# Kernel tuning notes

Hardware: AMD Instinct MI355X
Metric: run time of the kernel (lower is better)

## Reference

```python
import jax, jax.numpy as jnp
import numpy as np

# ---- constants derived from init_kwargs ----
DETECT_THRESHOLD = 3.0
DETECT_SIGN = -1          # negative spikes
MARGIN_LEFT = 20          # snippet_T1
MARGIN_RIGHT = 20         # snippet_T2
CHANNEL_RADIUS = 100.0
SAMPLING_FREQUENCY = 30000.0
TIME_RADIUS = int(np.ceil(0.5 / 1000.0 * SAMPLING_FREQUENCY))  # = 15
MAX_DETECTIONS = 100000   # static cap for jit-compatible compaction


def setup_inputs() -> dict:
    key = jax.random.key(0)
    k1, k2 = jax.random.split(key)
    traces = jax.random.normal(k1, (150000, 384), dtype=jnp.float32)
    # spread channels over a 2000x2000 um area so radius=100 gives sparse adjacency
    channel_locations = jax.random.uniform(k2, (384, 2), dtype=jnp.float32) * 2000.0
    return {"traces": traces, "channel_locations": channel_locations}


def _detect_mask(traces, channel_locations):
    N, M = traces.shape
    # orientation (detect_sign < 0 -> traces_inv = -traces)
    if DETECT_SIGN > 0:
        traces_inv = traces
    elif DETECT_SIGN == 0:
        traces_inv = jnp.abs(traces)
    else:
        traces_inv = -traces

    # temporal max-pool, kernel 2*TR+1, stride 1, same padding (pads with -inf)
    pool = 2 * TIME_RADIUS + 1
    neg_inf = jnp.float32(-jnp.inf)
    temporal_max = jax.lax.reduce_window(
        traces_inv, neg_inf, jax.lax.max,
        window_dimensions=(pool, 1), window_strides=(1, 1),
        padding=((TIME_RADIUS, TIME_RADIUS), (0, 0)))  # [N, M]

    # channel adjacency from pairwise distances
    diff = channel_locations[:, None, :] - channel_locations[None, :, :]
    dists = jnp.sqrt(jnp.sum(diff * diff, axis=-1))  # [M, M]
    adj = dists <= CHANNEL_RADIUS

    # per-channel masked neighbor max over temporal_max columns -> [N, M]
    # sequential lax.map over channels avoids an N x M x M intermediate
    spatial_max = jax.lax.map(
        lambda row: jnp.max(jnp.where(row[None, :], temporal_max, neg_inf), axis=1),
        adj).T  # [N, M]

    t = jnp.arange(N)
    margin_ok = (t >= MARGIN_LEFT) & (t < N - MARGIN_RIGHT)  # [N]

    valid = ((traces_inv == temporal_max)
             & (traces_inv >= DETECT_THRESHOLD)
             & margin_ok[:, None]
             & (traces_inv >= spatial_max))
    return valid, traces_inv


def reference(traces, channel_locations):
    valid, _ = _detect_mask(traces, channel_locations)
    # row-major nonzero order == stable sort by time (row index)
    times, chans = jnp.nonzero(valid, size=MAX_DETECTIONS, fill_value=-1)
    return times.astype(jnp.int64), chans.astype(jnp.int32)
```

## Files before the change

### kernel.cpp

```cpp
#include <hip/hip_runtime.h>
#include <stdint.h>

#define M_CH       384
#define TR         15
#define MARGIN     20
#define CHUNK_ROWS 16
#define BM_WORDS   192
#define WPR        12

__device__ __forceinline__ uint32_t spread4(uint32_t x) {
    x = (x | (x << 12)) & 0x000F000Fu;
    x = (x | (x << 6))  & 0x03030303u;
    x = (x | (x << 3))  & 0x11111111u;
    return x;
}

__global__ void nbr_kernel(const float* __restrict__ locs,
                           uint32_t* __restrict__ nEntries,
                           uint8_t* __restrict__ entryWord,
                           uint32_t* __restrict__ entryMask) {
    __shared__ float lx[M_CH], ly[M_CH];
    int t = threadIdx.x;
    lx[t] = locs[2 * t];
    ly[t] = locs[2 * t + 1];
    __syncthreads();
    float x = lx[t], y = ly[t];
    uint32_t m[WPR];
    #pragma unroll
    for (int k = 0; k < WPR; ++k) m[k] = 0;
    for (int c = 0; c < M_CH; ++c) {
        float dx = x - lx[c], dy = y - ly[c];
        if (sqrtf(dx * dx + dy * dy) <= 100.0f) m[c >> 5] |= 1u << (c & 31);
    }
    int ne = 0;
    #pragma unroll
    for (int k = 0; k < WPR; ++k) {
        if (m[k]) {
            entryWord[t * WPR + ne] = (uint8_t)k;
            entryMask[t * WPR + ne] = m[k];
            ne++;
        }
    }
    nEntries[t] = (uint32_t)ne;
}

__global__ __launch_bounds__(256)
void cand_kernel(const float* __restrict__ traces, long n4, long nwords,
                 uint32_t* __restrict__ candWords) {
    const int lane = threadIdx.x & 63;
    const long stride = (long)gridDim.x * 256;
    for (long i = (long)blockIdx.x * 256 + threadIdx.x; i - lane < n4; i += stride) {
        float4 v = make_float4(0.f, 0.f, 0.f, 0.f);
        if (i < n4) v = ((const float4*)traces)[i];
        uint64_t B0 = __ballot(v.x <= -3.0f);
        uint64_t B1 = __ballot(v.y <= -3.0f);
        uint64_t B2 = __ballot(v.z <= -3.0f);
        uint64_t B3 = __ballot(v.w <= -3.0f);
        if (lane < 8) {
            uint32_t b0 = (uint32_t)(B0 >> (8 * lane)) & 0xFFu;
            uint32_t b1 = (uint32_t)(B1 >> (8 * lane)) & 0xFFu;
            uint32_t b2 = (uint32_t)(B2 >> (8 * lane)) & 0xFFu;
            uint32_t b3 = (uint32_t)(B3 >> (8 * lane)) & 0xFFu;
            uint32_t word = spread4(b0) | (spread4(b1) << 1)
                          | (spread4(b2) << 2) | (spread4(b3) << 3);
            long wIdx = (i - lane) / 8 + lane;
            if (wIdx < nwords) candWords[wIdx] = word;
        }
    }
}

__global__ __launch_bounds__(256)
void validate_kernel(const float* __restrict__ traces, int N, long nwords,
                     const uint32_t* __restrict__ nEntries,
                     const uint8_t* __restrict__ entryWord,
                     const uint32_t* __restrict__ entryMask,
                     const uint32_t* __restrict__ candWords,
                     uint32_t* __restrict__ validOut) {
    long w = (long)blockIdx.x * 256 + threadIdx.x;
    if (w >= nwords) return;
    uint32_t word = candWords[w];
    uint32_t out = 0;
    if (word) {
        int r  = (int)(w / WPR);
        int cw = (int)(w - (long)r * WPR);
        if (r >= MARGIN && r < N - MARGIN) {
            out = word;
            uint32_t tmp = word;
            while (tmp) {
                int bit = __ffs(tmp) - 1;
                tmp &= tmp - 1;
                int c = cw * 32 + bit;
                float raw = traces[(long)r * M_CH + c];
                int ne = (int)nEntries[c];
                bool bad = false;
                for (int k = 0; k < ne; ++k) {
                    int wi = (int)entryWord[c * WPR + k];
                    uint32_t em = entryMask[c * WPR + k];
                    const uint32_t* colp = candWords + (long)(r - TR) * WPR + wi;
                    uint32_t hitRows = 0;
                    #pragma unroll
                    for (int dt = 0; dt < 31; ++dt) {
                        uint32_t h = colp[(long)dt * WPR] & em;
                        hitRows |= (h ? 1u : 0u) << dt;
                    }
                    if (hitRows) {
                        while (hitRows) {
                            int dt = __ffs(hitRows) - 1;
                            hitRows &= hitRows - 1;
                            uint32_t h = colp[(long)dt * WPR] & em;
                            while (h) {
                                int b2 = __ffs(h) - 1;
                                h &= h - 1;
                                float v = traces[(long)(r - TR + dt) * M_CH + wi * 32 + b2];
                                if (v < raw) bad = true;
                            }
                        }
                        if (bad) break;
                    }
                }
                if (bad) out &= ~(1u << bit);
            }
        }
    }
    validOut[w] = out;
}

__global__ void count_kernel(const uint32_t* __restrict__ validOut, int nchunk,
                             uint32_t* __restrict__ chunkCounts) {
    int lane  = threadIdx.x & 63;
    int chunk = (blockIdx.x * blockDim.x + threadIdx.x) >> 6;
    if (chunk >= nchunk) return;
    const uint32_t* wp = validOut + (long)chunk * BM_WORDS;
    int s = __popc(wp[lane]) + __popc(wp[lane + 64]) + __popc(wp[lane + 128]);
    #pragma unroll
    for (int off = 32; off; off >>= 1) s += __shfl_xor(s, off, 64);
    if (lane == 0) chunkCounts[chunk] = (uint32_t)s;
}

__global__ void scan_kernel(const uint32_t* __restrict__ counts, int n,
                            uint32_t* __restrict__ prefix) {
    __shared__ uint32_t s[256];
    int t = threadIdx.x;
    int per = (n + 255) / 256;
    int lo = t * per, hi = min(lo + per, n);
    uint32_t sum = 0;
    for (int i = lo; i < hi; ++i) sum += counts[i];
    s[t] = sum;
    __syncthreads();
    for (int off = 1; off < 256; off <<= 1) {
        uint32_t v = (t >= off) ? s[t - off] : 0;
        __syncthreads();
        s[t] += v;
        __syncthreads();
    }
    uint32_t run = s[t] - sum;
    for (int i = lo; i < hi; ++i) { prefix[i] = run; run += counts[i]; }
    if (t == 255) prefix[n] = run;
}

__global__ void emit_kernel(const uint32_t* __restrict__ validOut,
                            const uint32_t* __restrict__ chunkPrefix,
                            int nchunk, int maxdet,
                            int* __restrict__ times, int* __restrict__ chans) {
    int wv = threadIdx.x >> 6;
    int lane = threadIdx.x & 63;
    int chunkId = blockIdx.x * 4 + wv;
    if (chunkId >= nchunk) return;

    const uint32_t* wp = validOut + (long)chunkId * BM_WORDS + lane * 3;
    uint32_t b0 = wp[0], b1 = wp[1], b2 = wp[2];
    int local = __popc(b0) + __popc(b1) + __popc(b2);

    int s = local;
    #pragma unroll
    for (int off = 1; off < 64; off <<= 1) {
        int v = __shfl_up(s, off, 64);
        if (lane >= off) s += v;
    }
    int base = (int)chunkPrefix[chunkId] + (s - local);
    int r0 = chunkId * CHUNK_ROWS;

    uint32_t words[3] = { b0, b1, b2 };
    #pragma unroll
    for (int q = 0; q < 3; ++q) {
        uint32_t x = words[q];
        int fbase = (lane * 3 + q) * 32;
        while (x) {
            int b = __ffs(x) - 1;
            x &= x - 1;
            int f = fbase + b;
            int n = f / M_CH;
            int ch = f - n * M_CH;
            if (base < maxdet) {
                times[base] = r0 + n;
                chans[base] = ch;
            }
            base++;
        }
    }
}

__global__ void fill_kernel(const uint32_t* __restrict__ totalPtr, int maxdet,
                            int* __restrict__ times, int* __restrict__ chans) {
    int i = blockIdx.x * blockDim.x + threadIdx.x;
    int total = (int)*totalPtr;
    if (i < maxdet && i >= total) { times[i] = -1; chans[i] = -1; }
}

extern "C" void kernel_launch(void* const* d_in, const int* in_sizes, int n_in,
                              void* d_out, int out_size, void* d_ws, size_t ws_size,
                              hipStream_t stream) {
    const float* traces = (const float*)d_in[0];
    const float* locs   = (const float*)d_in[1];
    const int M = M_CH;
    const int N = in_sizes[0] / M;
    const long nsamp = (long)N * M;
    const int maxdet = out_size / 2;
    int* times = (int*)d_out;
    int* chans = times + maxdet;

    const long n4     = nsamp / 4;
    const long nwords = nsamp / 32;
    const int  nchunk = (N + CHUNK_ROWS - 1) / CHUNK_ROWS;

    char* ws = (char*)d_ws;
    uint32_t* nEntries    = (uint32_t*)(ws + 0);
    uint8_t*  entryWord   = (uint8_t*)(ws + 1536);
    uint32_t* entryMask   = (uint32_t*)(ws + 6144);
    uint32_t* chunkCounts = (uint32_t*)(ws + 24576);
    uint32_t* chunkPrefix = (uint32_t*)(ws + 62080);
    uint32_t* candWords   = (uint32_t*)(ws + 99584);
    uint32_t* validOut    = (uint32_t*)(ws + 7299584);

    nbr_kernel<<<1, M_CH, 0, stream>>>(locs, nEntries, entryWord, entryMask);

    cand_kernel<<<2048, 256, 0, stream>>>(traces, n4, nwords, candWords);

    validate_kernel<<<(int)((nwords + 255) / 256), 256, 0, stream>>>(
        traces, N, nwords, nEntries, entryWord, entryMask, candWords, validOut);

    count_kernel<<<(nchunk * 64 + 255) / 256, 256, 0, stream>>>(validOut, nchunk,
                                                                chunkCounts);

    scan_kernel<<<1, 256, 0, stream>>>(chunkCounts, nchunk, chunkPrefix);

    emit_kernel<<<(nchunk + 3) / 4, 256, 0, stream>>>(validOut, chunkPrefix,
                                                      nchunk, maxdet,
                                                      times, chans);

    fill_kernel<<<(maxdet + 255) / 256, 256, 0, stream>>>(chunkPrefix + nchunk,
                                                          maxdet, times, chans);
}
```

Before: 428.1 us.

## Fuse validate with chunk counting, emit with fill, and widen cand_kernel loads

The per-chunk popcount is folded into the validate kernel, which now runs one 192-thread block per 16-row chunk and reduces counts in shared memory. The fill pass is merged into the emit kernel as extra blocks. The candidate kernel switches from a grid-stride loop to one pass per wave that issues four float4 loads before balloting. Together these drop two kernel launches and one re-read of validOut, at the cost of smaller validate blocks and one more barrier.

```diff
diff --git a/kernel.cpp b/kernel.cpp
--- a/kernel.cpp
+++ b/kernel.cpp
@@ -48,93 +48,109 @@
 void cand_kernel(const float* __restrict__ traces, long n4, long nwords,
                  uint32_t* __restrict__ candWords) {
     const int lane = threadIdx.x & 63;
-    const long stride = (long)gridDim.x * 256;
-    for (long i = (long)blockIdx.x * 256 + threadIdx.x; i - lane < n4; i += stride) {
-        float4 v = make_float4(0.f, 0.f, 0.f, 0.f);
-        if (i < n4) v = ((const float4*)traces)[i];
-        uint64_t B0 = __ballot(v.x <= -3.0f);
-        uint64_t B1 = __ballot(v.y <= -3.0f);
-        uint64_t B2 = __ballot(v.z <= -3.0f);
-        uint64_t B3 = __ballot(v.w <= -3.0f);
-        if (lane < 8) {
-            uint32_t b0 = (uint32_t)(B0 >> (8 * lane)) & 0xFFu;
-            uint32_t b1 = (uint32_t)(B1 >> (8 * lane)) & 0xFFu;
-            uint32_t b2 = (uint32_t)(B2 >> (8 * lane)) & 0xFFu;
-            uint32_t b3 = (uint32_t)(B3 >> (8 * lane)) & 0xFFu;
-            uint32_t word = spread4(b0) | (spread4(b1) << 1)
-                          | (spread4(b2) << 2) | (spread4(b3) << 3);
-            long wIdx = (i - lane) / 8 + lane;
-            if (wIdx < nwords) candWords[wIdx] = word;
-        }
-    }
-}
-
-__global__ __launch_bounds__(256)
-void validate_kernel(const float* __restrict__ traces, int N, long nwords,
-                     const uint32_t* __restrict__ nEntries,
-                     const uint8_t* __restrict__ entryWord,
-                     const uint32_t* __restrict__ entryMask,
-                     const uint32_t* __restrict__ candWords,
-                     uint32_t* __restrict__ validOut) {
-    long w = (long)blockIdx.x * 256 + threadIdx.x;
-    if (w >= nwords) return;
-    uint32_t word = candWords[w];
+    const long wv = (((long)blockIdx.x * 256) + threadIdx.x) >> 6;
+    const long fb = wv * 256;
+    uint64_t B00,B01,B02,B03, B10,B11,B12,B13,
+             B20,B21,B22,B23, B30,B31,B32,B33;
+    {
+        float4 v0 = make_float4(0,0,0,0), v1 = v0, v2 = v0, v3 = v0;
+        long i0 = fb + 0 * 64 + lane;
+        long i1 = fb + 1 * 64 + lane;
+        long i2 = fb + 2 * 64 + lane;
+        long i3 = fb + 3 * 64 + lane;
+        if (i0 < n4) v0 = ((const float4*)traces)[i0];
+        if (i1 < n4) v1 = ((const float4*)traces)[i1];
+        if (i2 < n4) v2 = ((const float4*)traces)[i2];
+        if (i3 < n4) v3 = ((const float4*)traces)[i3];
+        B00 = __ballot(v0.x <= -3.0f); B01 = __ballot(v0.y <= -3.0f);
+        B02 = __ballot(v0.z <= -3.0f); B03 = __ballot(v0.w <= -3.0f);
+        B10 = __ballot(v1.x <= -3.0f); B11 = __ballot(v1.y <= -3.0f);
+        B12 = __ballot(v1.z <= -3.0f); B13 = __ballot(v1.w <= -3.0f);
+        B20 = __ballot(v2.x <= -3.0f); B21 = __ballot(v2.y <= -3.0f);
+        B22 = __ballot(v2.z <= -3.0f); B23 = __ballot(v2.w <= -3.0f);
+        B30 = __ballot(v3.x <= -3.0f); B31 = __ballot(v3.y <= -3.0f);
+        B32 = __ballot(v3.z <= -3.0f); B33 = __ballot(v3.w <= -3.0f);
+    }
+    if (lane < 32) {
+        int k  = lane >> 3;
+        int sh = (lane & 7) * 8;
+        uint64_t b0 = (k & 2) ? ((k & 1) ? B30 : B20) : ((k & 1) ? B10 : B00);
+        uint64_t b1 = (k & 2) ? ((k & 1) ? B31 : B21) : ((k & 1) ? B11 : B01);
+        uint64_t b2 = (k & 2) ? ((k & 1) ? B32 : B22) : ((k & 1) ? B12 : B02);
+        uint64_t b3 = (k & 2) ? ((k & 1) ? B33 : B23) : ((k & 1) ? B13 : B03);
+        uint32_t w = spread4((uint32_t)(b0 >> sh) & 0xFFu)
+                   | (spread4((uint32_t)(b1 >> sh) & 0xFFu) << 1)
+                   | (spread4((uint32_t)(b2 >> sh) & 0xFFu) << 2)
+                   | (spread4((uint32_t)(b3 >> sh) & 0xFFu) << 3);
+        long wIdx = wv * 32 + lane;
+        if (wIdx < nwords) candWords[wIdx] = w;
+    }
+}
+
+__global__ __launch_bounds__(192)
+void validate_count_kernel(const float* __restrict__ traces, int N, long nwords,
+                           const uint32_t* __restrict__ nEntries,
+                           const uint8_t* __restrict__ entryWord,
+                           const uint32_t* __restrict__ entryMask,
+                           const uint32_t* __restrict__ candWords,
+                           uint32_t* __restrict__ validOut,
+                           uint32_t* __restrict__ chunkCounts) {
+    __shared__ uint32_t red[3];
+    const int t = threadIdx.x;
+    const long w = (long)blockIdx.x * BM_WORDS + t;
     uint32_t out = 0;
-    if (word) {
-        int r  = (int)(w / WPR);
-        int cw = (int)(w - (long)r * WPR);
-        if (r >= MARGIN && r < N - MARGIN) {
-            out = word;
-            uint32_t tmp = word;
-            while (tmp) {
-                int bit = __ffs(tmp) - 1;
-                tmp &= tmp - 1;
-                int c = cw * 32 + bit;
-                float raw = traces[(long)r * M_CH + c];
-                int ne = (int)nEntries[c];
-                bool bad = false;
-                for (int k = 0; k < ne; ++k) {
-                    int wi = (int)entryWord[c * WPR + k];
-                    uint32_t em = entryMask[c * WPR + k];
-                    const uint32_t* colp = candWords + (long)(r - TR) * WPR + wi;
-                    uint32_t hitRows = 0;
-                    #pragma unroll
-                    for (int dt = 0; dt < 31; ++dt) {
-                        uint32_t h = colp[(long)dt * WPR] & em;
-                        hitRows |= (h ? 1u : 0u) << dt;
+    if (w < nwords) {
+        uint32_t word = candWords[w];
+        if (word) {
+            int r  = (int)(w / WPR);
+            int cw = (int)(w - (long)r * WPR);
+            if (r >= MARGIN && r < N - MARGIN) {
+                out = word;
+                uint32_t tmp = word;
+                while (tmp) {
+                    int bit = __ffs(tmp) - 1;
+                    tmp &= tmp - 1;
+                    int c = cw * 32 + bit;
+                    float raw = traces[(long)r * M_CH + c];
+                    int ne = (int)nEntries[c];
+                    bool bad = false;
+                    for (int k = 0; k < ne; ++k) {
+                        int wi = (int)entryWord[c * WPR + k];
+                        uint32_t em = entryMask[c * WPR + k];
+                        const uint32_t* colp = candWords + (long)(r - TR) * WPR + wi;
+                        uint32_t hitRows = 0;
+                        #pragma unroll
+                        for (int dt = 0; dt < 31; ++dt) {
+                            uint32_t h = colp[(long)dt * WPR] & em;
+                            hitRows |= (h ? 1u : 0u) << dt;
+                        }
+                        if (hitRows) {
+                            while (hitRows) {
+                                int dt = __ffs(hitRows) - 1;
+                                hitRows &= hitRows - 1;
+                                uint32_t h = colp[(long)dt * WPR] & em;
+                                while (h) {
+                                    int b2 = __ffs(h) - 1;
+                                    h &= h - 1;
+                                    float v = traces[(long)(r - TR + dt) * M_CH + wi * 32 + b2];
+                                    if (v < raw) bad = true;
+                                }
+                            }
+                            if (bad) break;
+                        }
                     }
-                    if (hitRows) {
-                        while (hitRows) {
-                            int dt = __ffs(hitRows) - 1;
-                            hitRows &= hitRows - 1;
-                            uint32_t h = colp[(long)dt * WPR] & em;
-                            while (h) {
-                                int b2 = __ffs(h) - 1;
-                                h &= h - 1;
-                                float v = traces[(long)(r - TR + dt) * M_CH + wi * 32 + b2];
-                                if (v < raw) bad = true;
-                            }
-                        }
-                        if (bad) break;
-                    }
+                    if (bad) out &= ~(1u << bit);
                 }
-                if (bad) out &= ~(1u << bit);
             }
         }
-    }
-    validOut[w] = out;
-}
-
-__global__ void count_kernel(const uint32_t* __restrict__ validOut, int nchunk,
-                             uint32_t* __restrict__ chunkCounts) {
-    int lane  = threadIdx.x & 63;
-    int chunk = (blockIdx.x * blockDim.x + threadIdx.x) >> 6;
-    if (chunk >= nchunk) return;
-    const uint32_t* wp = validOut + (long)chunk * BM_WORDS;
-    int s = __popc(wp[lane]) + __popc(wp[lane + 64]) + __popc(wp[lane + 128]);
-    #pragma unroll
-    for (int off = 32; off; off >>= 1) s += __shfl_xor(s, off, 64);
-    if (lane == 0) chunkCounts[chunk] = (uint32_t)s;
+        validOut[w] = out;
+    }
+    int pc = __popc(out);
+    #pragma unroll
+    for (int off = 32; off; off >>= 1) pc += __shfl_xor(pc, off, 64);
+    if ((t & 63) == 0) red[t >> 6] = (uint32_t)pc;
+    __syncthreads();
+    if (t == 0) chunkCounts[blockIdx.x] = red[0] + red[1] + red[2];
 }
 
 __global__ void scan_kernel(const uint32_t* __restrict__ counts, int n,
@@ -158,10 +174,16 @@
     if (t == 255) prefix[n] = run;
 }
 
-__global__ void emit_kernel(const uint32_t* __restrict__ validOut,
-                            const uint32_t* __restrict__ chunkPrefix,
-                            int nchunk, int maxdet,
-                            int* __restrict__ times, int* __restrict__ chans) {
+__global__ void emit_fill_kernel(const uint32_t* __restrict__ validOut,
+                                 const uint32_t* __restrict__ chunkPrefix,
+                                 int nchunk, int emitBlocks, int maxdet,
+                                 int* __restrict__ times, int* __restrict__ chans) {
+    if ((int)blockIdx.x >= emitBlocks) {
+        int i = ((int)blockIdx.x - emitBlocks) * 256 + threadIdx.x;
+        int total = (int)chunkPrefix[nchunk];
+        if (i < maxdet && i >= total) { times[i] = -1; chans[i] = -1; }
+        return;
+    }
     int wv = threadIdx.x >> 6;
     int lane = threadIdx.x & 63;
     int chunkId = blockIdx.x * 4 + wv;
@@ -200,13 +222,6 @@
     }
 }
 
-__global__ void fill_kernel(const uint32_t* __restrict__ totalPtr, int maxdet,
-                            int* __restrict__ times, int* __restrict__ chans) {
-    int i = blockIdx.x * blockDim.x + threadIdx.x;
-    int total = (int)*totalPtr;
-    if (i < maxdet && i >= total) { times[i] = -1; chans[i] = -1; }
-}
-
 extern "C" void kernel_launch(void* const* d_in, const int* in_sizes, int n_in,
                               void* d_out, int out_size, void* d_ws, size_t ws_size,
                               hipStream_t stream) {
@@ -234,20 +249,18 @@
 
     nbr_kernel<<<1, M_CH, 0, stream>>>(locs, nEntries, entryWord, entryMask);
 
-    cand_kernel<<<2048, 256, 0, stream>>>(traces, n4, nwords, candWords);
-
-    validate_kernel<<<(int)((nwords + 255) / 256), 256, 0, stream>>>(
-        traces, N, nwords, nEntries, entryWord, entryMask, candWords, validOut);
-
-    count_kernel<<<(nchunk * 64 + 255) / 256, 256, 0, stream>>>(validOut, nchunk,
-                                                                chunkCounts);
+    const long nwaves = (nwords + 31) / 32;
+    const int  cblocks = (int)((nwaves + 3) / 4);
+    cand_kernel<<<cblocks, 256, 0, stream>>>(traces, n4, nwords, candWords);
+
+    validate_count_kernel<<<nchunk, BM_WORDS, 0, stream>>>(
+        traces, N, nwords, nEntries, entryWord, entryMask, candWords,
+        validOut, chunkCounts);
 
     scan_kernel<<<1, 256, 0, stream>>>(chunkCounts, nchunk, chunkPrefix);
 
-    emit_kernel<<<(nchunk + 3) / 4, 256, 0, stream>>>(validOut, chunkPrefix,
-                                                      nchunk, maxdet,
-                                                      times, chans);
-
-    fill_kernel<<<(maxdet + 255) / 256, 256, 0, stream>>>(chunkPrefix + nchunk,
-                                                          maxdet, times, chans);
-}
+    const int emitBlocks = (nchunk + 3) / 4;
+    const int fillBlocks = (maxdet + 255) / 256;
+    emit_fill_kernel<<<emitBlocks + fillBlocks, 256, 0, stream>>>(
+        validOut, chunkPrefix, nchunk, emitBlocks, maxdet, times, chans);
+}
```

New measurement: 425.6 us. Within noise of the previous version (-0.6%).
